# Kernel optimization log

Measured on AMD Instinct MI355X. Metric: run time of the kernel, lower is better.

The kernel has to match this reference:

```python
import jax, jax.numpy as jnp
import numpy as np

B, CIN, COUT, G = 1, 64, 64, 1
NLAT, NLON = 256, 512
LMAX, MMAX = NLAT, NLON // 2 + 1  # torch-harmonics: lmax=nlat, mmax=nlon//2+1


def _legpoly(mmax, lmax, cost):
    """Fully (ortho) normalized associated Legendre \bar P_l^m(cos t), shape [mmax, lmax, nlat]."""
    nlat = cost.shape[0]
    p = np.zeros((mmax, lmax, nlat), dtype=np.float64)
    sint = np.sqrt(1.0 - cost * cost)
    pmm = np.full(nlat, np.sqrt(1.0 / (4.0 * np.pi)))  # \bar P_0^0
    for m in range(mmax):
        if m < lmax:
            p[m, m] = pmm
        if m + 1 < lmax:
            p[m, m + 1] = np.sqrt(2.0 * m + 3.0) * cost * pmm
        for l in range(m + 2, lmax):
            a = np.sqrt((4.0 * l * l - 1.0) / (l * l - m * m))
            b = np.sqrt(((l - 1.0) ** 2 - m * m) / (4.0 * (l - 1.0) ** 2 - 1.0))
            p[m, l] = a * (cost * p[m, l - 1] - b * p[m, l - 2])
        # diagonal step: \bar P_{m+1}^{m+1}
        pmm = -np.sqrt((2.0 * m + 3.0) / (2.0 * m + 2.0)) * sint * pmm
    return p


def setup_inputs():
    key = jax.random.key(0)
    k1, k2, k3 = jax.random.split(key, 3)
    # Gauss-Legendre nodes/weights (grid='legendre-gauss')
    cost, wq = np.polynomial.legendre.leggauss(NLAT)
    pct = _legpoly(MMAX, LMAX, cost)                      # [m, l, k] - ISHT matrix
    sht_w = pct * wq[None, None, :]                        # [m, l, k] - SHT matrix (Legendre * quadrature)
    x = jax.random.normal(k1, (B, CIN, NLAT, NLON), jnp.float32)
    # weight init: scale = sqrt(1/(Cin/g)), scale[0] *= sqrt(2); complex randn has var 1/2 per component
    scale = np.full(LMAX, np.sqrt(1.0 / (CIN // G)), np.float32)
    scale[0] *= np.sqrt(2.0)
    scale = scale * np.sqrt(0.5)
    weight_r = jax.random.normal(k2, (G, CIN // G, COUT // G, LMAX), jnp.float32) * scale
    weight_i = jax.random.normal(k3, (G, CIN // G, COUT // G, LMAX), jnp.float32) * scale
    return {"x": x, "weight_r": weight_r, "weight_i": weight_i,
            "pct": jnp.asarray(pct.astype(np.float32)),
            "sht_w": jnp.asarray(sht_w.astype(np.float32))}


def reference(x, weight_r, weight_i, pct, sht_w):
    residual = x  # scale_residual is False (same in/out shape and grid)
    x = x.astype(jnp.float32)
    # --- forward real SHT: rfft over lon, Legendre transform over lat ---
    xf = 2.0 * jnp.pi * jnp.fft.rfft(x, axis=-1, norm="forward")          # [B,C,k,m] complex64
    coeffs = jnp.einsum('bckm,mlk->bclm', xf, sht_w.astype(xf.dtype))      # [B,C,l,m]
    Bd, C, L, M = coeffs.shape
    # --- grouped per-l complex weight contraction (_contract_lwise) ---
    w = (weight_r + 1j * weight_i).astype(coeffs.dtype)                    # [g,i,o,l]
    xg = coeffs.reshape(Bd, G, C // G, L, M)
    out = jnp.einsum('bgilm,giol->bgolm', xg, w).reshape(Bd, COUT, L, M)
    # --- inverse real SHT ---
    xk = jnp.einsum('bolm,mlk->bokm', out, pct.astype(out.dtype))          # [B,Cout,k,m]
    y = jnp.fft.irfft(xk, n=NLON, axis=-1, norm="forward")                 # [B,Cout,nlat,nlon]
    return (y.astype(residual.dtype), residual)
```

## Files before the change

### kernel.cpp

```cpp
#include <hip/hip_runtime.h>

typedef _Float16 f16;
typedef _Float16 h8 __attribute__((ext_vector_type(8)));
typedef float f4 __attribute__((ext_vector_type(4)));

#define NLON 512
#define NLAT 256
#define NC   64
#define NM   256
#define NL   256
#define RTOT (NC*NLAT)

#define BO_FTR 0
#define BO_FTI (BO_FTR + 262144)
#define BO_GR  (BO_FTI + 262144)
#define BO_GI  (BO_GR  + 262144)
#define BO_WTR (BO_GI  + 262144)
#define BO_WTI (BO_WTR + 2097152)
#define BO_XFRE (BO_WTI + 2097152)
#define BO_XFIM (BO_XFRE + 8388608)
#define BO_PRE  (BO_XFIM + 8388608)
#define BO_PIM  (BO_PRE + 8388608)
#define BO_QRE  (BO_PIM + 8388608)
#define BO_QIM  (BO_QRE + 8388608)
// ... 14 lines not shown
    const float sc = 6.2831853071795864769f / 512.0f;
    Ftr[idx] = (f16)(sc * cosf(th));
    Fti[idx] = (f16)(-sc * sinf(th));
  }
  {
    int n = idx >> 8, m = idx & 255;
    int t = (n * m) & (NLON - 1);
    float th = t * step;
    float s = (m == 0) ? 1.0f : 2.0f;
    Gr[idx] = (f16)(s * cosf(th));
    Gi[idx] = (f16)(-s * sinf(th));
  }
}

__global__ void k_permw2(const float* __restrict__ wr, const float* __restrict__ wi,
                         f16* __restrict__ wTr, f16* __restrict__ wTi) {
  __shared__ float tile[32][33];
  int z = blockIdx.z;
  int o = z >> 1;
  const float* w = (z & 1) ? wi : wr;
  f16* wT = (z & 1) ? wTi : wTr;
  int i0 = blockIdx.y * 32;
  int l0 = blockIdx.x * 32;
  int xx = threadIdx.x, yy = threadIdx.y;
  for (int j = 0; j < 32; j += 8)
    tile[yy + j][xx] = w[(size_t)(i0 + yy + j) * (NC * NL) + (size_t)o * NL + l0 + xx];
  __syncthreads();
  for (int j = 0; j < 32; j += 8)
    wT[(size_t)(l0 + yy + j) * (NC * NC) + (size_t)o * NC + i0 + xx] = (f16)tile[xx][yy + j];
}

__global__ __launch_bounds__(256) void k_s1(
    const float* __restrict__ x, const f16* __restrict__ Ftr,
    const f16* __restrict__ Fti, f16* __restrict__ XFre, f16* __restrict__ XFim,
    float* __restrict__ res) {
  __shared__ f16 Ar[128 * 40], Ai[128 * 40], Bx[64 * 40];
  int t = threadIdx.x;
  int m0 = blockIdx.x * 128, r0 = blockIdx.y * 64;
  int lane = t & 63, w = t >> 6;
  int wm = (w >> 1) * 32, wn = (w & 1) * 32;
  int fr = lane & 15, kg = (lane >> 4) * 8;
  int srow = t >> 2, skc = (t & 3) * 8;
  f4 aR[4][2] = {}, aI[4][2] = {};
  for (int n0 = 0; n0 < NLON; n0 += 32) {
#pragma unroll
    for (int rep = 0; rep < 2; ++rep) {
      int f = rep * 256 + t;
      int row = f >> 2, c8 = (f & 3) * 8;
      *(h8*)&Ar[row * 40 + c8] = *(const h8*)(Ftr + (size_t)(m0 + row) * NLON + n0 + c8);
      *(h8*)&Ai[row * 40 + c8] = *(const h8*)(Fti + (size_t)(m0 + row) * NLON + n0 + c8);
    }
    const float* px = x + (size_t)(r0 + srow) * NLON + n0 + skc;
    float4 v0 = *(const float4*)px;
    float4 v1 = *(const float4*)(px + 4);
    if (blockIdx.x == 0) {
      float* pr = res + (size_t)(r0 + srow) * NLON + n0 + skc;
      *(float4*)pr = v0;
      *(float4*)(pr + 4) = v1;
    }
    h8 hx = {(f16)v0.x, (f16)v0.y, (f16)v0.z, (f16)v0.w,
             (f16)v1.x, (f16)v1.y, (f16)v1.z, (f16)v1.w};
    *(h8*)&Bx[srow * 40 + skc] = hx;
    __syncthreads();
    h8 b0 = *(h8*)&Bx[(wn + fr) * 40 + kg];
    h8 b1 = *(h8*)&Bx[(wn + 16 + fr) * 40 + kg];
#pragma unroll
    for (int im = 0; im < 4; ++im) {
      int mrow = wm + (im >> 1) * 64 + (im & 1) * 16 + fr;
      h8 a = *(h8*)&Ar[mrow * 40 + kg];
      h8 c = *(h8*)&Ai[mrow * 40 + kg];
      aR[im][0] = mfma16(a, b0, aR[im][0]); aR[im][1] = mfma16(a, b1, aR[im][1]);
      aI[im][0] = mfma16(c, b0, aI[im][0]); aI[im][1] = mfma16(c, b1, aI[im][1]);
    }
    __syncthreads();
  }
  int drow = (lane >> 4) * 4, dcol = lane & 15;
#pragma unroll
  for (int im = 0; im < 4; ++im)
#pragma unroll
    for (int j = 0; j < 2; ++j)
#pragma unroll
      for (int b = 0; b < 4; ++b) {
        int mg = m0 + wm + (im >> 1) * 64 + (im & 1) * 16 + drow + b;
        size_t o = (size_t)mg * RTOT + r0 + wn + j * 16 + dcol;
        XFre[o] = (f16)aR[im][j][b];
        XFim[o] = (f16)aI[im][j][b];
      }
}

__global__ __launch_bounds__(256) void k_s2(
    const f16* __restrict__ XFre, const f16* __restrict__ XFim,
    const float* __restrict__ shtw, f16* __restrict__ Pre, f16* __restrict__ Pim) {
  int m = blockIdx.y;
  int l0 = blockIdx.x * 64;
  int t = threadIdx.x;
  if (l0 + 64 <= m) {
    h8 z = {};
#pragma unroll
    for (int rep = 0; rep < 2; ++rep) {
      int f = rep * 256 + t;
      int ll = f >> 3, c8 = (f & 7) * 8;
      size_t o = (size_t)(l0 + ll) * RTOT + (size_t)m * 64 + c8;
      *(h8*)(Pre + o) = z;
      *(h8*)(Pim + o) = z;
    }
    return;
  }
  __shared__ f16 SH[9216];
  f16* Ar = SH;
  f16* Ai = SH + 2560;
  f16* Bs = SH + 5120;
  int lane = t & 63, w = t >> 6;
  int wm = (w >> 1) * 32, wn = (w & 1) * 32;
  int fr = lane & 15, kg = (lane >> 4) * 8;
  int srow = t >> 2, skc = (t & 3) * 8;
  const f16* Abr = XFre + (size_t)m * RTOT;
  const f16* Abi = XFim + (size_t)m * RTOT;
  const float* Bb = shtw + (size_t)m * (NL * NLAT);
  f4 aR[2][2] = {}, aI[2][2] = {};
  for (int k0 = 0; k0 < NLAT; k0 += 32) {
    *(h8*)&Ar[srow * 40 + skc] = *(const h8*)(Abr + (size_t)srow * NLAT + k0 + skc);
    *(h8*)&Ai[srow * 40 + skc] = *(const h8*)(Abi + (size_t)srow * NLAT + k0 + skc);
    const float* pb = Bb + (size_t)(l0 + srow) * NLAT + k0 + skc;
    float4 v0 = *(const float4*)pb;
    float4 v1 = *(const float4*)(pb + 4);
    h8 hb = {(f16)v0.x, (f16)v0.y, (f16)v0.z, (f16)v0.w,
             (f16)v1.x, (f16)v1.y, (f16)v1.z, (f16)v1.w};
    *(h8*)&Bs[srow * 40 + skc] = hb;
    __syncthreads();
    h8 a0 = *(h8*)&Ar[(wm + fr) * 40 + kg],      a1 = *(h8*)&Ar[(wm + 16 + fr) * 40 + kg];
    h8 c0 = *(h8*)&Ai[(wm + fr) * 40 + kg],      c1 = *(h8*)&Ai[(wm + 16 + fr) * 40 + kg];
    h8 b0 = *(h8*)&Bs[(wn + fr) * 40 + kg],      b1 = *(h8*)&Bs[(wn + 16 + fr) * 40 + kg];
    aR[0][0] = mfma16(a0, b0, aR[0][0]); aR[0][1] = mfma16(a0, b1, aR[0][1]);
    aR[1][0] = mfma16(a1, b0, aR[1][0]); aR[1][1] = mfma16(a1, b1, aR[1][1]);
    aI[0][0] = mfma16(c0, b0, aI[0][0]); aI[0][1] = mfma16(c0, b1, aI[0][1]);
    aI[1][0] = mfma16(c1, b0, aI[1][0]); aI[1][1] = mfma16(c1, b1, aI[1][1]);
    __syncthreads();
  }
  f16* Tr = SH;
  f16* Ti = SH + 4608;
  int drow = (lane >> 4) * 4, dcol = lane & 15;
#pragma unroll
  for (int i = 0; i < 2; ++i)
#pragma unroll
    for (int j = 0; j < 2; ++j)
#pragma unroll
      for (int b = 0; b < 4; ++b) {
        int c = wm + i * 16 + drow + b;
        int l = wn + j * 16 + dcol;
        Tr[l * 72 + c] = (f16)aR[i][j][b];
        Ti[l * 72 + c] = (f16)aI[i][j][b];
      }
  __syncthreads();
#pragma unroll
  for (int rep = 0; rep < 4; ++rep) {
    int f = rep * 256 + t;
    int buf = f >> 9, idx = f & 511;
    int ll = idx >> 3, c8 = (idx & 7) * 8;
    const f16* T = buf ? Ti : Tr;
    h8 v = *(const h8*)&T[ll * 72 + c8];
    f16* Pd = buf ? Pim : Pre;
    *(h8*)(Pd + (size_t)(l0 + ll) * RTOT + (size_t)m * 64 + c8) = v;
  }
}

__global__ __launch_bounds__(256) void k_s3(
    const f16* __restrict__ Pre, const f16* __restrict__ Pim,
    const f16* __restrict__ wTr, const f16* __restrict__ wTi,
    f16* __restrict__ Qre, f16* __restrict__ Qim) {
  int l = blockIdx.y;
  int m0 = blockIdx.x * 64;
  int t = threadIdx.x;
  size_t obase = (size_t)l * RTOT + (size_t)m0 * 64;
  if (m0 > l) {
    h8 z = {};
#pragma unroll
    for (int rep = 0; rep < 2; ++rep) {
      int f = rep * 256 + t;
      ((h8*)(Qre + obase))[f] = z;
      ((h8*)(Qim + obase))[f] = z;
    }
    return;
  }
  __shared__ f16 SH[18432];
  f16* Ar = SH;
  f16* Ai = SH + 4608;
  f16* Br = SH + 9216;
  f16* Bi = SH + 13824;
  const f16* Pbr = Pre + (size_t)l * RTOT + (size_t)m0 * 64;
  const f16* Pbi = Pim + (size_t)l * RTOT + (size_t)m0 * 64;
  const f16* Wbr = wTr + (size_t)l * 4096;
  const f16* Wbi = wTi + (size_t)l * 4096;
#pragma unroll
  for (int rep = 0; rep < 2; ++rep) {
    int f = rep * 256 + t;
    int row = f >> 3, c8 = (f & 7) * 8;
    *(h8*)&Ar[row * 72 + c8] = *(const h8*)(Pbr + (size_t)row * 64 + c8);
    *(h8*)&Ai[row * 72 + c8] = *(const h8*)(Pbi + (size_t)row * 64 + c8);
    *(h8*)&Br[row * 72 + c8] = *(const h8*)(Wbr + (size_t)f * 8);
    *(h8*)&Bi[row * 72 + c8] = *(const h8*)(Wbi + (size_t)f * 8);
  }
  __syncthreads();
  int lane = t & 63, w = t >> 6;
  int wm = (w >> 1) * 32, wn = (w & 1) * 32;
  int fr = lane & 15, kg = (lane >> 4) * 8;
  f4 RR[2][2] = {}, II[2][2] = {}, RI[2][2] = {}, IR[2][2] = {};
#pragma unroll
  for (int ks = 0; ks < 64; ks += 32) {
    h8 a0 = *(h8*)&Ar[(wm + fr) * 72 + ks + kg];
    h8 a1 = *(h8*)&Ar[(wm + 16 + fr) * 72 + ks + kg];
    h8 c0 = *(h8*)&Ai[(wm + fr) * 72 + ks + kg];
    h8 c1 = *(h8*)&Ai[(wm + 16 + fr) * 72 + ks + kg];
    h8 b0 = *(h8*)&Br[(wn + fr) * 72 + ks + kg];
    h8 b1 = *(h8*)&Br[(wn + 16 + fr) * 72 + ks + kg];
    h8 d0 = *(h8*)&Bi[(wn + fr) * 72 + ks + kg];
    h8 d1 = *(h8*)&Bi[(wn + 16 + fr) * 72 + ks + kg];
// ... 7 lines not shown
    IR[1][0] = mfma16(c1, b0, IR[1][0]); IR[1][1] = mfma16(c1, b1, IR[1][1]);
  }
  __syncthreads();
  f16* Tr = SH;
  f16* Ti = SH + 4608;
  int drow = (lane >> 4) * 4, dcol = lane & 15;
#pragma unroll
  for (int i = 0; i < 2; ++i)
#pragma unroll
    for (int j = 0; j < 2; ++j)
#pragma unroll
      for (int b = 0; b < 4; ++b) {
        int mm = wm + i * 16 + drow + b;
        int oo = wn + j * 16 + dcol;
        Tr[mm * 72 + oo] = (f16)(RR[i][j][b] - II[i][j][b]);
        Ti[mm * 72 + oo] = (f16)(RI[i][j][b] + IR[i][j][b]);
      }
  __syncthreads();
#pragma unroll
  for (int rep = 0; rep < 4; ++rep) {
    int f = rep * 256 + t;
    int buf = f >> 9, idx = f & 511;
    int mm = idx >> 3, o8 = (idx & 7) * 8;
    const f16* T = buf ? Ti : Tr;
    h8 v = *(const h8*)&T[mm * 72 + o8];
    f16* Qd = buf ? Qim : Qre;
    *(h8*)(Qd + obase + (size_t)mm * 64 + o8) = v;
  }
}

__global__ __launch_bounds__(256) void k_s4(
    const f16* __restrict__ Qre, const f16* __restrict__ Qim,
    const float* __restrict__ pct, f16* __restrict__ XKre, f16* __restrict__ XKim) {
  __shared__ f16 As[32 * 66], Ais[32 * 66], Bs0[32 * 66], Bs1[32 * 66];
  int m = blockIdx.y;
  int k0b = blockIdx.x * 128;
  int t = threadIdx.x;
  int lane = t & 63, w = t >> 6;
  int wm = (w >> 1) * 32, wn = (w & 1) * 32;
  int fr = lane & 15, kg = (lane >> 4) * 8;
  int lr = t >> 3, c8 = (t & 7) * 8;
  const float* Bb = pct + (size_t)m * (NL * NLAT);
  f4 aR[2][4] = {}, aI[2][4] = {};
  int lstart = m & ~31;
  for (int l0 = lstart; l0 < NL; l0 += 32) {
    *(h8*)&As[lr * 66 + c8]  = *(const h8*)(Qre + (size_t)(l0 + lr) * RTOT + (size_t)m * 64 + c8);
    *(h8*)&Ais[lr * 66 + c8] = *(const h8*)(Qim + (size_t)(l0 + lr) * RTOT + (size_t)m * 64 + c8);
    const float* pb = Bb + (size_t)(l0 + lr) * NLAT + k0b + c8;
    {
      float4 v0 = *(const float4*)pb;
      float4 v1 = *(const float4*)(pb + 4);
      h8 hb = {(f16)v0.x, (f16)v0.y, (f16)v0.z, (f16)v0.w,
               (f16)v1.x, (f16)v1.y, (f16)v1.z, (f16)v1.w};
      *(h8*)&Bs0[lr * 66 + c8] = hb;
    }
    {
      float4 v0 = *(const float4*)(pb + 64);
      float4 v1 = *(const float4*)(pb + 68);
      h8 hb = {(f16)v0.x, (f16)v0.y, (f16)v0.z, (f16)v0.w,
               (f16)v1.x, (f16)v1.y, (f16)v1.z, (f16)v1.w};
      *(h8*)&Bs1[lr * 66 + c8] = hb;
    }
    __syncthreads();
    h8 a0, a1, c0, c1, b0, b1, b2, b3;
#pragma unroll
    for (int e = 0; e < 8; ++e) {
      int row = (kg + e) * 66;
      a0[e] = As[row + wm + fr];
      a1[e] = As[row + wm + 16 + fr];
      c0[e] = Ais[row + wm + fr];
      c1[e] = Ais[row + wm + 16 + fr];
      b0[e] = Bs0[row + wn + fr];
      b1[e] = Bs0[row + wn + 16 + fr];
      b2[e] = Bs1[row + wn + fr];
      b3[e] = Bs1[row + wn + 16 + fr];
    }
    aR[0][0] = mfma16(a0, b0, aR[0][0]); aR[0][1] = mfma16(a0, b1, aR[0][1]);
    aR[0][2] = mfma16(a0, b2, aR[0][2]); aR[0][3] = mfma16(a0, b3, aR[0][3]);
    aR[1][0] = mfma16(a1, b0, aR[1][0]); aR[1][1] = mfma16(a1, b1, aR[1][1]);
    aR[1][2] = mfma16(a1, b2, aR[1][2]); aR[1][3] = mfma16(a1, b3, aR[1][3]);
    aI[0][0] = mfma16(c0, b0, aI[0][0]); aI[0][1] = mfma16(c0, b1, aI[0][1]);
    aI[0][2] = mfma16(c0, b2, aI[0][2]); aI[0][3] = mfma16(c0, b3, aI[0][3]);
    aI[1][0] = mfma16(c1, b0, aI[1][0]); aI[1][1] = mfma16(c1, b1, aI[1][1]);
    aI[1][2] = mfma16(c1, b2, aI[1][2]); aI[1][3] = mfma16(c1, b3, aI[1][3]);
    __syncthreads();
  }
  int drow = (lane >> 4) * 4, dcol = lane & 15;
#pragma unroll
  for (int i = 0; i < 2; ++i)
#pragma unroll
    for (int j = 0; j < 4; ++j)
#pragma unroll
      for (int b = 0; b < 4; ++b) {
        int orow = wm + i * 16 + drow + b;
        int kcol = k0b + (j >> 1) * 64 + (j & 1) * 16 + wn + dcol;
        size_t o = (size_t)m * RTOT + (size_t)orow * NLAT + kcol;
        XKre[o] = (f16)aR[i][j][b];
        XKim[o] = (f16)aI[i][j][b];
      }
}

__global__ __launch_bounds__(256) void k_s5(
    const f16* __restrict__ XKre, const f16* __restrict__ XKim,
    const f16* __restrict__ Gr, const f16* __restrict__ Gi,
    float* __restrict__ y) {
  __shared__ f16 Ar[32 * 66], Ai[32 * 66], Br[128 * 34], Bi[128 * 34];
  int t = threadIdx.x;
  int n0 = blockIdx.x * 128, r0 = blockIdx.y * 64;
  int lane = t & 63, w = t >> 6;
  int wm = (w >> 1) * 32, wn = (w & 1) * 32;
  int fr = lane & 15, kg = (lane >> 4) * 8;
  int mr = t >> 3, r8 = (t & 7) * 8;
  f4 acc[2][4] = {};
  for (int m0 = 0; m0 < NM; m0 += 32) {
    *(h8*)&Ar[mr * 66 + r8] = *(const h8*)(XKre + (size_t)(m0 + mr) * RTOT + r0 + r8);
    *(h8*)&Ai[mr * 66 + r8] = *(const h8*)(XKim + (size_t)(m0 + mr) * RTOT + r0 + r8);
#pragma unroll
    for (int rep = 0; rep < 2; ++rep) {
      int f = rep * 256 + t;
      int row = f >> 2, cc = (f & 3) * 8;
      *(h8*)&Br[row * 34 + cc] = *(const h8*)(Gr + (size_t)(n0 + row) * NM + m0 + cc);
      *(h8*)&Bi[row * 34 + cc] = *(const h8*)(Gi + (size_t)(n0 + row) * NM + m0 + cc);
    }
    __syncthreads();
    h8 a0, a1, c0, c1;
#pragma unroll
    for (int e = 0; e < 8; ++e) {
      int row = (kg + e) * 66;
      a0[e] = Ar[row + wm + fr];
      a1[e] = Ar[row + wm + 16 + fr];
      c0[e] = Ai[row + wm + fr];
      c1[e] = Ai[row + wm + 16 + fr];
    }
#pragma unroll
    for (int j = 0; j < 4; ++j) {
      int nb = wn + (j & 1) * 16 + (j >> 1) * 64;
      h8 b = *(h8*)&Br[(nb + fr) * 34 + kg];
      h8 d = *(h8*)&Bi[(nb + fr) * 34 + kg];
      acc[0][j] = mfma16(a0, b, acc[0][j]);
      acc[1][j] = mfma16(a1, b, acc[1][j]);
      acc[0][j] = mfma16(c0, d, acc[0][j]);
      acc[1][j] = mfma16(c1, d, acc[1][j]);
    }
    __syncthreads();
  }
  int drow = (lane >> 4) * 4, dcol = lane & 15;
#pragma unroll
  for (int i = 0; i < 2; ++i)
#pragma unroll
    for (int j = 0; j < 4; ++j)
#pragma unroll
      for (int b = 0; b < 4; ++b) {
        int rg = r0 + wm + i * 16 + drow + b;
        int ng = n0 + wn + (j & 1) * 16 + (j >> 1) * 64 + dcol;
        y[(size_t)rg * NLON + ng] = acc[i][j][b];
      }
}

extern "C" void kernel_launch(void* const* d_in, const int* in_sizes, int n_in,
                              void* d_out, int out_size, void* d_ws, size_t ws_size,
                              hipStream_t stream) {
  const float* x    = (const float*)d_in[0];
  const float* wgr  = (const float*)d_in[1];
  const float* wgi  = (const float*)d_in[2];
  const float* pct  = (const float*)d_in[3];
  const float* shtw = (const float*)d_in[4];
  float* out = (float*)d_out;
  char* ws = (char*)d_ws;

  f16* Ftr = (f16*)(ws + BO_FTR);
  f16* Fti = (f16*)(ws + BO_FTI);
  f16* Gr  = (f16*)(ws + BO_GR);
  f16* Gi  = (f16*)(ws + BO_GI);
  f16* wTr = (f16*)(ws + BO_WTR);
  f16* wTi = (f16*)(ws + BO_WTI);
  f16* XFre = (f16*)(ws + BO_XFRE);
  f16* XFim = (f16*)(ws + BO_XFIM);
  f16* Pre  = (f16*)(ws + BO_PRE);
  f16* Pim  = (f16*)(ws + BO_PIM);
  f16* Qre  = (f16*)(ws + BO_QRE);
  f16* Qim  = (f16*)(ws + BO_QIM);

  float* res = out + (size_t)NC * NLAT * NLON;

  hipLaunchKernelGGL(k_tables_h, dim3(512), dim3(256), 0, stream, Ftr, Fti, Gr, Gi);
  hipLaunchKernelGGL(k_permw2, dim3(8, 2, 128), dim3(32, 8), 0, stream, wgr, wgi, wTr, wTi);
  hipLaunchKernelGGL(k_s1, dim3(2, 256), dim3(256), 0, stream, x, Ftr, Fti, XFre, XFim, res);
  hipLaunchKernelGGL(k_s2, dim3(4, 256), dim3(256), 0, stream, XFre, XFim, shtw, Pre, Pim);
  hipLaunchKernelGGL(k_s3, dim3(4, 256), dim3(256), 0, stream, Pre, Pim, wTr, wTi, Qre, Qim);
  hipLaunchKernelGGL(k_s4, dim3(2, 256), dim3(256), 0, stream, Qre, Qim, pct, XFre, XFim);
  hipLaunchKernelGGL(k_s5, dim3(4, 256), dim3(256), 0, stream, XFre, XFim, Gr, Gi, out);
}
```

Baseline: 117.0 us.

## Double-buffer shared memory with register prefetch in four GEMM stage kernels

Stages s1, s2, s4 and s5 now keep two shared-memory tile buffers. Each one loads the next K-slice from global memory into registers while MFMAs run on the current buffer, then writes the prefetched data into the other buffer. This halves the __syncthreads per iteration and is meant to hide global load latency behind compute. In exchange it doubles LDS usage and raises register pressure, which may lower occupancy.

```diff
diff --git a/kernel.cpp b/kernel.cpp
--- a/kernel.cpp
+++ b/kernel.cpp
@@ -72,45 +72,86 @@
     const float* __restrict__ x, const f16* __restrict__ Ftr,
     const f16* __restrict__ Fti, f16* __restrict__ XFre, f16* __restrict__ XFim,
     float* __restrict__ res) {
-  __shared__ f16 Ar[128 * 40], Ai[128 * 40], Bx[64 * 40];
+  __shared__ f16 SH[2 * 12800];
   int t = threadIdx.x;
   int m0 = blockIdx.x * 128, r0 = blockIdx.y * 64;
   int lane = t & 63, w = t >> 6;
   int wm = (w >> 1) * 32, wn = (w & 1) * 32;
   int fr = lane & 15, kg = (lane >> 4) * 8;
   int srow = t >> 2, skc = (t & 3) * 8;
+  int arow0 = t >> 2, ac = (t & 3) * 8;
+  int arow1 = (t + 256) >> 2;
   f4 aR[4][2] = {}, aI[4][2] = {};
-  for (int n0 = 0; n0 < NLON; n0 += 32) {
-#pragma unroll
-    for (int rep = 0; rep < 2; ++rep) {
-      int f = rep * 256 + t;
-      int row = f >> 2, c8 = (f & 3) * 8;
-      *(h8*)&Ar[row * 40 + c8] = *(const h8*)(Ftr + (size_t)(m0 + row) * NLON + n0 + c8);
-      *(h8*)&Ai[row * 40 + c8] = *(const h8*)(Fti + (size_t)(m0 + row) * NLON + n0 + c8);
-    }
-    const float* px = x + (size_t)(r0 + srow) * NLON + n0 + skc;
-    float4 v0 = *(const float4*)px;
-    float4 v1 = *(const float4*)(px + 4);
+  h8 rAr0, rAr1, rAi0, rAi1;
+  float4 rX0, rX1;
+  rAr0 = *(const h8*)(Ftr + (size_t)(m0 + arow0) * NLON + ac);
+  rAr1 = *(const h8*)(Ftr + (size_t)(m0 + arow1) * NLON + ac);
+  rAi0 = *(const h8*)(Fti + (size_t)(m0 + arow0) * NLON + ac);
+  rAi1 = *(const h8*)(Fti + (size_t)(m0 + arow1) * NLON + ac);
+  {
+    const float* px = x + (size_t)(r0 + srow) * NLON + skc;
+    rX0 = *(const float4*)px; rX1 = *(const float4*)(px + 4);
     if (blockIdx.x == 0) {
-      float* pr = res + (size_t)(r0 + srow) * NLON + n0 + skc;
-      *(float4*)pr = v0;
-      *(float4*)(pr + 4) = v1;
-    }
-    h8 hx = {(f16)v0.x, (f16)v0.y, (f16)v0.z, (f16)v0.w,
-             (f16)v1.x, (f16)v1.y, (f16)v1.z, (f16)v1.w};
+      float* pr = res + (size_t)(r0 + srow) * NLON + skc;
+      *(float4*)pr = rX0; *(float4*)(pr + 4) = rX1;
+    }
+  }
+  {
+    f16* Ar = SH; f16* Ai = SH + 5120; f16* Bx = SH + 10240;
+    *(h8*)&Ar[arow0 * 40 + ac] = rAr0;
+    *(h8*)&Ar[arow1 * 40 + ac] = rAr1;
+    *(h8*)&Ai[arow0 * 40 + ac] = rAi0;
+    *(h8*)&Ai[arow1 * 40 + ac] = rAi1;
+    h8 hx = {(f16)rX0.x, (f16)rX0.y, (f16)rX0.z, (f16)rX0.w,
+             (f16)rX1.x, (f16)rX1.y, (f16)rX1.z, (f16)rX1.w};
     *(h8*)&Bx[srow * 40 + skc] = hx;
+  }
+  __syncthreads();
+  int cur = 0;
+  for (int it = 0; it < 16; ++it) {
+    bool more = (it + 1) < 16;
+    if (more) {
+      int n0 = (it + 1) * 32;
+      rAr0 = *(const h8*)(Ftr + (size_t)(m0 + arow0) * NLON + n0 + ac);
+      rAr1 = *(const h8*)(Ftr + (size_t)(m0 + arow1) * NLON + n0 + ac);
+      rAi0 = *(const h8*)(Fti + (size_t)(m0 + arow0) * NLON + n0 + ac);
+      rAi1 = *(const h8*)(Fti + (size_t)(m0 + arow1) * NLON + n0 + ac);
+      const float* px = x + (size_t)(r0 + srow) * NLON + n0 + skc;
+      rX0 = *(const float4*)px; rX1 = *(const float4*)(px + 4);
+      if (blockIdx.x == 0) {
+        float* pr = res + (size_t)(r0 + srow) * NLON + n0 + skc;
+        *(float4*)pr = rX0; *(float4*)(pr + 4) = rX1;
+      }
+    }
+    {
+      const f16* Ar = SH + cur * 12800;
+      const f16* Ai = Ar + 5120;
+      const f16* Bx = Ar + 10240;
+      h8 b0 = *(const h8*)&Bx[(wn + fr) * 40 + kg];
+      h8 b1 = *(const h8*)&Bx[(wn + 16 + fr) * 40 + kg];
+#pragma unroll
+      for (int im = 0; im < 4; ++im) {
+        int mrow = wm + (im >> 1) * 64 + (im & 1) * 16 + fr;
+        h8 a = *(const h8*)&Ar[mrow * 40 + kg];
+        h8 c = *(const h8*)&Ai[mrow * 40 + kg];
+        aR[im][0] = mfma16(a, b0, aR[im][0]); aR[im][1] = mfma16(a, b1, aR[im][1]);
+        aI[im][0] = mfma16(c, b0, aI[im][0]); aI[im][1] = mfma16(c, b1, aI[im][1]);
+      }
+    }
+    if (more) {
+      f16* Ar = SH + (cur ^ 1) * 12800;
+      f16* Ai = Ar + 5120;
+      f16* Bx = Ar + 10240;
+      *(h8*)&Ar[arow0 * 40 + ac] = rAr0;
+      *(h8*)&Ar[arow1 * 40 + ac] = rAr1;
+      *(h8*)&Ai[arow0 * 40 + ac] = rAi0;
+      *(h8*)&Ai[arow1 * 40 + ac] = rAi1;
+      h8 hx = {(f16)rX0.x, (f16)rX0.y, (f16)rX0.z, (f16)rX0.w,
+               (f16)rX1.x, (f16)rX1.y, (f16)rX1.z, (f16)rX1.w};
+      *(h8*)&Bx[srow * 40 + skc] = hx;
+    }
     __syncthreads();
-    h8 b0 = *(h8*)&Bx[(wn + fr) * 40 + kg];
-    h8 b1 = *(h8*)&Bx[(wn + 16 + fr) * 40 + kg];
-#pragma unroll
-    for (int im = 0; im < 4; ++im) {
-      int mrow = wm + (im >> 1) * 64 + (im & 1) * 16 + fr;
-      h8 a = *(h8*)&Ar[mrow * 40 + kg];
-      h8 c = *(h8*)&Ai[mrow * 40 + kg];
-      aR[im][0] = mfma16(a, b0, aR[im][0]); aR[im][1] = mfma16(a, b1, aR[im][1]);
-      aI[im][0] = mfma16(c, b0, aI[im][0]); aI[im][1] = mfma16(c, b1, aI[im][1]);
-    }
-    __syncthreads();
+    cur ^= 1;
   }
   int drow = (lane >> 4) * 4, dcol = lane & 15;
 #pragma unroll
@@ -130,24 +171,21 @@
     const f16* __restrict__ XFre, const f16* __restrict__ XFim,
     const float* __restrict__ shtw, f16* __restrict__ Pre, f16* __restrict__ Pim) {
   int m = blockIdx.y;
-  int l0 = blockIdx.x * 64;
+  int l0b = blockIdx.x * 64;
   int t = threadIdx.x;
-  if (l0 + 64 <= m) {
+  if (l0b + 64 <= m) {
     h8 z = {};
 #pragma unroll
     for (int rep = 0; rep < 2; ++rep) {
       int f = rep * 256 + t;
       int ll = f >> 3, c8 = (f & 7) * 8;
-      size_t o = (size_t)(l0 + ll) * RTOT + (size_t)m * 64 + c8;
+      size_t o = (size_t)(l0b + ll) * RTOT + (size_t)m * 64 + c8;
       *(h8*)(Pre + o) = z;
       *(h8*)(Pim + o) = z;
     }
     return;
   }
-  __shared__ f16 SH[9216];
-  f16* Ar = SH;
-  f16* Ai = SH + 2560;
-  f16* Bs = SH + 5120;
+  __shared__ f16 SH[2 * 7680];
   int lane = t & 63, w = t >> 6;
   int wm = (w >> 1) * 32, wn = (w & 1) * 32;
   int fr = lane & 15, kg = (lane >> 4) * 8;
@@ -156,24 +194,57 @@
   const f16* Abi = XFim + (size_t)m * RTOT;
   const float* Bb = shtw + (size_t)m * (NL * NLAT);
   f4 aR[2][2] = {}, aI[2][2] = {};
-  for (int k0 = 0; k0 < NLAT; k0 += 32) {
-    *(h8*)&Ar[srow * 40 + skc] = *(const h8*)(Abr + (size_t)srow * NLAT + k0 + skc);
-    *(h8*)&Ai[srow * 40 + skc] = *(const h8*)(Abi + (size_t)srow * NLAT + k0 + skc);
-    const float* pb = Bb + (size_t)(l0 + srow) * NLAT + k0 + skc;
-    float4 v0 = *(const float4*)pb;
-    float4 v1 = *(const float4*)(pb + 4);
-    h8 hb = {(f16)v0.x, (f16)v0.y, (f16)v0.z, (f16)v0.w,
-             (f16)v1.x, (f16)v1.y, (f16)v1.z, (f16)v1.w};
+  h8 rA, rAi;
+  float4 rB0, rB1;
+  rA  = *(const h8*)(Abr + (size_t)srow * NLAT + skc);
+  rAi = *(const h8*)(Abi + (size_t)srow * NLAT + skc);
+  {
+    const float* pb = Bb + (size_t)(l0b + srow) * NLAT + skc;
+    rB0 = *(const float4*)pb; rB1 = *(const float4*)(pb + 4);
+  }
+  {
+    f16* Ar = SH; f16* Ai = SH + 2560; f16* Bs = SH + 5120;
+    *(h8*)&Ar[srow * 40 + skc] = rA;
+    *(h8*)&Ai[srow * 40 + skc] = rAi;
+    h8 hb = {(f16)rB0.x, (f16)rB0.y, (f16)rB0.z, (f16)rB0.w,
+             (f16)rB1.x, (f16)rB1.y, (f16)rB1.z, (f16)rB1.w};
     *(h8*)&Bs[srow * 40 + skc] = hb;
+  }
+  __syncthreads();
+  int cur = 0;
+  for (int it = 0; it < 8; ++it) {
+    bool more = (it + 1) < 8;
+    if (more) {
+      int k0 = (it + 1) * 32;
+      rA  = *(const h8*)(Abr + (size_t)srow * NLAT + k0 + skc);
+      rAi = *(const h8*)(Abi + (size_t)srow * NLAT + k0 + skc);
+      const float* pb = Bb + (size_t)(l0b + srow) * NLAT + k0 + skc;
+      rB0 = *(const float4*)pb; rB1 = *(const float4*)(pb + 4);
+    }
+    {
+      const f16* Ar = SH + cur * 7680;
+      const f16* Ai = Ar + 2560;
+      const f16* Bs = Ar + 5120;
+      h8 a0 = *(const h8*)&Ar[(wm + fr) * 40 + kg],      a1 = *(const h8*)&Ar[(wm + 16 + fr) * 40 + kg];
+      h8 c0 = *(const h8*)&Ai[(wm + fr) * 40 + kg],      c1 = *(const h8*)&Ai[(wm + 16 + fr) * 40 + kg];
+      h8 b0 = *(const h8*)&Bs[(wn + fr) * 40 + kg],      b1 = *(const h8*)&Bs[(wn + 16 + fr) * 40 + kg];
+      aR[0][0] = mfma16(a0, b0, aR[0][0]); aR[0][1] = mfma16(a0, b1, aR[0][1]);
+      aR[1][0] = mfma16(a1, b0, aR[1][0]); aR[1][1] = mfma16(a1, b1, aR[1][1]);
+      aI[0][0] = mfma16(c0, b0, aI[0][0]); aI[0][1] = mfma16(c0, b1, aI[0][1]);
+      aI[1][0] = mfma16(c1, b0, aI[1][0]); aI[1][1] = mfma16(c1, b1, aI[1][1]);
+    }
+    if (more) {
+      f16* Ar = SH + (cur ^ 1) * 7680;
+      f16* Ai = Ar + 2560;
+      f16* Bs = Ar + 5120;
+      *(h8*)&Ar[srow * 40 + skc] = rA;
+      *(h8*)&Ai[srow * 40 + skc] = rAi;
+      h8 hb = {(f16)rB0.x, (f16)rB0.y, (f16)rB0.z, (f16)rB0.w,
+               (f16)rB1.x, (f16)rB1.y, (f16)rB1.z, (f16)rB1.w};
+      *(h8*)&Bs[srow * 40 + skc] = hb;
+    }
     __syncthreads();
-    h8 a0 = *(h8*)&Ar[(wm + fr) * 40 + kg],      a1 = *(h8*)&Ar[(wm + 16 + fr) * 40 + kg];
-    h8 c0 = *(h8*)&Ai[(wm + fr) * 40 + kg],      c1 = *(h8*)&Ai[(wm + 16 + fr) * 40 + kg];
-    h8 b0 = *(h8*)&Bs[(wn + fr) * 40 + kg],      b1 = *(h8*)&Bs[(wn + 16 + fr) * 40 + kg];
-    aR[0][0] = mfma16(a0, b0, aR[0][0]); aR[0][1] = mfma16(a0, b1, aR[0][1]);
-    aR[1][0] = mfma16(a1, b0, aR[1][0]); aR[1][1] = mfma16(a1, b1, aR[1][1]);
-    aI[0][0] = mfma16(c0, b0, aI[0][0]); aI[0][1] = mfma16(c0, b1, aI[0][1]);
-    aI[1][0] = mfma16(c1, b0, aI[1][0]); aI[1][1] = mfma16(c1, b1, aI[1][1]);
-    __syncthreads();
+    cur ^= 1;
   }
   f16* Tr = SH;
   f16* Ti = SH + 4608;
@@ -198,7 +269,7 @@
     const f16* T = buf ? Ti : Tr;
     h8 v = *(const h8*)&T[ll * 72 + c8];
     f16* Pd = buf ? Pim : Pre;
-    *(h8*)(Pd + (size_t)(l0 + ll) * RTOT + (size_t)m * 64 + c8) = v;
+    *(h8*)(Pd + (size_t)(l0b + ll) * RTOT + (size_t)m * 64 + c8) = v;
   }
 }
 
@@ -293,7 +364,7 @@
 __global__ __launch_bounds__(256) void k_s4(
     const f16* __restrict__ Qre, const f16* __restrict__ Qim,
     const float* __restrict__ pct, f16* __restrict__ XKre, f16* __restrict__ XKim) {
-  __shared__ f16 As[32 * 66], Ais[32 * 66], Bs0[32 * 66], Bs1[32 * 66];
+  __shared__ f16 SH[2 * 8448];
   int m = blockIdx.y;
   int k0b = blockIdx.x * 128;
   int t = threadIdx.x;
@@ -304,47 +375,82 @@
   const float* Bb = pct + (size_t)m * (NL * NLAT);
   f4 aR[2][4] = {}, aI[2][4] = {};
   int lstart = m & ~31;
-  for (int l0 = lstart; l0 < NL; l0 += 32) {
-    *(h8*)&As[lr * 66 + c8]  = *(const h8*)(Qre + (size_t)(l0 + lr) * RTOT + (size_t)m * 64 + c8);
-    *(h8*)&Ais[lr * 66 + c8] = *(const h8*)(Qim + (size_t)(l0 + lr) * RTOT + (size_t)m * 64 + c8);
-    const float* pb = Bb + (size_t)(l0 + lr) * NLAT + k0b + c8;
+  int nt = (NL - lstart) >> 5;
+  h8 rQr, rQi;
+  float4 rP0, rP1, rP2, rP3;
+  rQr = *(const h8*)(Qre + (size_t)(lstart + lr) * RTOT + (size_t)m * 64 + c8);
+  rQi = *(const h8*)(Qim + (size_t)(lstart + lr) * RTOT + (size_t)m * 64 + c8);
+  {
+    const float* pb = Bb + (size_t)(lstart + lr) * NLAT + k0b + c8;
+    rP0 = *(const float4*)pb;       rP1 = *(const float4*)(pb + 4);
+    rP2 = *(const float4*)(pb + 64); rP3 = *(const float4*)(pb + 68);
+  }
+  {
+    f16* As = SH; f16* Ais = SH + 2112; f16* Bs0 = SH + 4224; f16* Bs1 = SH + 6336;
+    *(h8*)&As[lr * 66 + c8] = rQr;
+    *(h8*)&Ais[lr * 66 + c8] = rQi;
+    h8 h0 = {(f16)rP0.x, (f16)rP0.y, (f16)rP0.z, (f16)rP0.w,
+             (f16)rP1.x, (f16)rP1.y, (f16)rP1.z, (f16)rP1.w};
+    h8 h1 = {(f16)rP2.x, (f16)rP2.y, (f16)rP2.z, (f16)rP2.w,
+             (f16)rP3.x, (f16)rP3.y, (f16)rP3.z, (f16)rP3.w};
+    *(h8*)&Bs0[lr * 66 + c8] = h0;
+    *(h8*)&Bs1[lr * 66 + c8] = h1;
+  }
+  __syncthreads();
+  int cur = 0;
+  for (int it = 0; it < nt; ++it) {
+    bool more = (it + 1) < nt;
+    if (more) {
+      int l0 = lstart + (it + 1) * 32;
+      rQr = *(const h8*)(Qre + (size_t)(l0 + lr) * RTOT + (size_t)m * 64 + c8);
+      rQi = *(const h8*)(Qim + (size_t)(l0 + lr) * RTOT + (size_t)m * 64 + c8);
+      const float* pb = Bb + (size_t)(l0 + lr) * NLAT + k0b + c8;
+      rP0 = *(const float4*)pb;       rP1 = *(const float4*)(pb + 4);
+      rP2 = *(const float4*)(pb + 64); rP3 = *(const float4*)(pb + 68);
+    }
     {
-      float4 v0 = *(const float4*)pb;
-      float4 v1 = *(const float4*)(pb + 4);
-      h8 hb = {(f16)v0.x, (f16)v0.y, (f16)v0.z, (f16)v0.w,
-               (f16)v1.x, (f16)v1.y, (f16)v1.z, (f16)v1.w};
-      *(h8*)&Bs0[lr * 66 + c8] = hb;
-    }
-    {
-      float4 v0 = *(const float4*)(pb + 64);
-      float4 v1 = *(const float4*)(pb + 68);
-      h8 hb = {(f16)v0.x, (f16)v0.y, (f16)v0.z, (f16)v0.w,
-               (f16)v1.x, (f16)v1.y, (f16)v1.z, (f16)v1.w};
-      *(h8*)&Bs1[lr * 66 + c8] = hb;
+      const f16* As = SH + cur * 8448;
+      const f16* Ais = As + 2112;
+      const f16* Bs0 = As + 4224;
+      const f16* Bs1 = As + 6336;
+      h8 a0, a1, c0, c1, b0, b1, b2, b3;
+#pragma unroll
+      for (int e = 0; e < 8; ++e) {
+        int row = (kg + e) * 66;
+        a0[e] = As[row + wm + fr];
+        a1[e] = As[row + wm + 16 + fr];
+        c0[e] = Ais[row + wm + fr];
+        c1[e] = Ais[row + wm + 16 + fr];
+        b0[e] = Bs0[row + wn + fr];
+        b1[e] = Bs0[row + wn + 16 + fr];
+        b2[e] = Bs1[row + wn + fr];
+        b3[e] = Bs1[row + wn + 16 + fr];
+      }
+      aR[0][0] = mfma16(a0, b0, aR[0][0]); aR[0][1] = mfma16(a0, b1, aR[0][1]);
+      aR[0][2] = mfma16(a0, b2, aR[0][2]); aR[0][3] = mfma16(a0, b3, aR[0][3]);
+      aR[1][0] = mfma16(a1, b0, aR[1][0]); aR[1][1] = mfma16(a1, b1, aR[1][1]);
+      aR[1][2] = mfma16(a1, b2, aR[1][2]); aR[1][3] = mfma16(a1, b3, aR[1][3]);
+      aI[0][0] = mfma16(c0, b0, aI[0][0]); aI[0][1] = mfma16(c0, b1, aI[0][1]);
+      aI[0][2] = mfma16(c0, b2, aI[0][2]); aI[0][3] = mfma16(c0, b3, aI[0][3]);
+      aI[1][0] = mfma16(c1, b0, aI[1][0]); aI[1][1] = mfma16(c1, b1, aI[1][1]);
+      aI[1][2] = mfma16(c1, b2, aI[1][2]); aI[1][3] = mfma16(c1, b3, aI[1][3]);
+    }
+    if (more) {
+      f16* As = SH + (cur ^ 1) * 8448;
+      f16* Ais = As + 2112;
+      f16* Bs0 = As + 4224;
+      f16* Bs1 = As + 6336;
+      *(h8*)&As[lr * 66 + c8] = rQr;
+      *(h8*)&Ais[lr * 66 + c8] = rQi;
+      h8 h0 = {(f16)rP0.x, (f16)rP0.y, (f16)rP0.z, (f16)rP0.w,
+               (f16)rP1.x, (f16)rP1.y, (f16)rP1.z, (f16)rP1.w};
+      h8 h1 = {(f16)rP2.x, (f16)rP2.y, (f16)rP2.z, (f16)rP2.w,
+               (f16)rP3.x, (f16)rP3.y, (f16)rP3.z, (f16)rP3.w};
+      *(h8*)&Bs0[lr * 66 + c8] = h0;
+      *(h8*)&Bs1[lr * 66 + c8] = h1;
     }
     __syncthreads();
-    h8 a0, a1, c0, c1, b0, b1, b2, b3;
-#pragma unroll
-    for (int e = 0; e < 8; ++e) {
-      int row = (kg + e) * 66;
-      a0[e] = As[row + wm + fr];
-      a1[e] = As[row + wm + 16 + fr];
-      c0[e] = Ais[row + wm + fr];
-      c1[e] = Ais[row + wm + 16 + fr];
-      b0[e] = Bs0[row + wn + fr];
-      b1[e] = Bs0[row + wn + 16 + fr];
-      b2[e] = Bs1[row + wn + fr];
-      b3[e] = Bs1[row + wn + 16 + fr];
-    }
-    aR[0][0] = mfma16(a0, b0, aR[0][0]); aR[0][1] = mfma16(a0, b1, aR[0][1]);
-    aR[0][2] = mfma16(a0, b2, aR[0][2]); aR[0][3] = mfma16(a0, b3, aR[0][3]);
-    aR[1][0] = mfma16(a1, b0, aR[1][0]); aR[1][1] = mfma16(a1, b1, aR[1][1]);
-    aR[1][2] = mfma16(a1, b2, aR[1][2]); aR[1][3] = mfma16(a1, b3, aR[1][3]);
-    aI[0][0] = mfma16(c0, b0, aI[0][0]); aI[0][1] = mfma16(c0, b1, aI[0][1]);
-    aI[0][2] = mfma16(c0, b2, aI[0][2]); aI[0][3] = mfma16(c0, b3, aI[0][3]);
-    aI[1][0] = mfma16(c1, b0, aI[1][0]); aI[1][1] = mfma16(c1, b1, aI[1][1]);
-    aI[1][2] = mfma16(c1, b2, aI[1][2]); aI[1][3] = mfma16(c1, b3, aI[1][3]);
-    __syncthreads();
+    cur ^= 1;
   }
   int drow = (lane >> 4) * 4, dcol = lane & 15;
 #pragma unroll
@@ -365,45 +471,84 @@
     const f16* __restrict__ XKre, const f16* __restrict__ XKim,
     const f16* __restrict__ Gr, const f16* __restrict__ Gi,
     float* __restrict__ y) {
-  __shared__ f16 Ar[32 * 66], Ai[32 * 66], Br[128 * 34], Bi[128 * 34];
+  __shared__ f16 SH[2 * 12928];
   int t = threadIdx.x;
   int n0 = blockIdx.x * 128, r0 = blockIdx.y * 64;
   int lane = t & 63, w = t >> 6;
   int wm = (w >> 1) * 32, wn = (w & 1) * 32;
   int fr = lane & 15, kg = (lane >> 4) * 8;
   int mr = t >> 3, r8 = (t & 7) * 8;
+  int brow0 = t >> 2, bc = (t & 3) * 8;
+  int brow1 = (t + 256) >> 2;
   f4 acc[2][4] = {};
-  for (int m0 = 0; m0 < NM; m0 += 32) {
-    *(h8*)&Ar[mr * 66 + r8] = *(const h8*)(XKre + (size_t)(m0 + mr) * RTOT + r0 + r8);
-    *(h8*)&Ai[mr * 66 + r8] = *(const h8*)(XKim + (size_t)(m0 + mr) * RTOT + r0 + r8);
-#pragma unroll
-    for (int rep = 0; rep < 2; ++rep) {
-      int f = rep * 256 + t;
-      int row = f >> 2, cc = (f & 3) * 8;
-      *(h8*)&Br[row * 34 + cc] = *(const h8*)(Gr + (size_t)(n0 + row) * NM + m0 + cc);
-      *(h8*)&Bi[row * 34 + cc] = *(const h8*)(Gi + (size_t)(n0 + row) * NM + m0 + cc);
+  h8 rXr, rXi, rG0, rG1, rH0, rH1;
+  rXr = *(const h8*)(XKre + (size_t)mr * RTOT + r0 + r8);
+  rXi = *(const h8*)(XKim + (size_t)mr * RTOT + r0 + r8);
+  rG0 = *(const h8*)(Gr + (size_t)(n0 + brow0) * NM + bc);
+  rG1 = *(const h8*)(Gr + (size_t)(n0 + brow1) * NM + bc);
+  rH0 = *(const h8*)(Gi + (size_t)(n0 + brow0) * NM + bc);
+  rH1 = *(const h8*)(Gi + (size_t)(n0 + brow1) * NM + bc);
+  {
+    f16* Ar = SH; f16* Ai = SH + 2112; f16* Br = SH + 4224; f16* Bi = SH + 8576;
+    *(h8*)&Ar[mr * 66 + r8] = rXr;
+    *(h8*)&Ai[mr * 66 + r8] = rXi;
+    *(h8*)&Br[brow0 * 34 + bc] = rG0;
+    *(h8*)&Br[brow1 * 34 + bc] = rG1;
+    *(h8*)&Bi[brow0 * 34 + bc] = rH0;
+    *(h8*)&Bi[brow1 * 34 + bc] = rH1;
+  }
+  __syncthreads();
+  int cur = 0;
+  for (int it = 0; it < 8; ++it) {
+    bool more = (it + 1) < 8;
+    if (more) {
+      int m0 = (it + 1) * 32;
+      rXr = *(const h8*)(XKre + (size_t)(m0 + mr) * RTOT + r0 + r8);
+      rXi = *(const h8*)(XKim + (size_t)(m0 + mr) * RTOT + r0 + r8);
+      rG0 = *(const h8*)(Gr + (size_t)(n0 + brow0) * NM + m0 + bc);
+      rG1 = *(const h8*)(Gr + (size_t)(n0 + brow1) * NM + m0 + bc);
+      rH0 = *(const h8*)(Gi + (size_t)(n0 + brow0) * NM + m0 + bc);
+      rH1 = *(const h8*)(Gi + (size_t)(n0 + brow1) * NM + m0 + bc);
+    }
+    {
+      const f16* Ar = SH + cur * 12928;
+      const f16* Ai = Ar + 2112;
+      const f16* Br = Ar + 4224;
+      const f16* Bi = Ar + 8576;
+      h8 a0, a1, c0, c1;
+#pragma unroll
+      for (int e = 0; e < 8; ++e) {
+        int row = (kg + e) * 66;
+        a0[e] = Ar[row + wm + fr];
+        a1[e] = Ar[row + wm + 16 + fr];
+        c0[e] = Ai[row + wm + fr];
+        c1[e] = Ai[row + wm + 16 + fr];
+      }
+#pragma unroll
+      for (int j = 0; j < 4; ++j) {
+        int nb = wn + (j & 1) * 16 + (j >> 1) * 64;
+        h8 b = *(const h8*)&Br[(nb + fr) * 34 + kg];
+        h8 d = *(const h8*)&Bi[(nb + fr) * 34 + kg];
+        acc[0][j] = mfma16(a0, b, acc[0][j]);
+        acc[1][j] = mfma16(a1, b, acc[1][j]);
+        acc[0][j] = mfma16(c0, d, acc[0][j]);
+        acc[1][j] = mfma16(c1, d, acc[1][j]);
+      }
+    }
+    if (more) {
+      f16* Ar = SH + (cur ^ 1) * 12928;
+      f16* Ai = Ar + 2112;
+      f16* Br = Ar + 4224;
+      f16* Bi = Ar + 8576;
+      *(h8*)&Ar[mr * 66 + r8] = rXr;
+      *(h8*)&Ai[mr * 66 + r8] = rXi;
+      *(h8*)&Br[brow0 * 34 + bc] = rG0;
+      *(h8*)&Br[brow1 * 34 + bc] = rG1;
+      *(h8*)&Bi[brow0 * 34 + bc] = rH0;
+      *(h8*)&Bi[brow1 * 34 + bc] = rH1;
     }
     __syncthreads();
-    h8 a0, a1, c0, c1;
-#pragma unroll
-    for (int e = 0; e < 8; ++e) {
-      int row = (kg + e) * 66;
-      a0[e] = Ar[row + wm + fr];
-      a1[e] = Ar[row + wm + 16 + fr];
-      c0[e] = Ai[row + wm + fr];
-      c1[e] = Ai[row + wm + 16 + fr];
-    }
-#pragma unroll
-    for (int j = 0; j < 4; ++j) {
-      int nb = wn + (j & 1) * 16 + (j >> 1) * 64;
-      h8 b = *(h8*)&Br[(nb + fr) * 34 + kg];
-      h8 d = *(h8*)&Bi[(nb + fr) * 34 + kg];
-      acc[0][j] = mfma16(a0, b, acc[0][j]);
-      acc[1][j] = mfma16(a1, b, acc[1][j]);
-      acc[0][j] = mfma16(c0, d, acc[0][j]);
-      acc[1][j] = mfma16(c1, d, acc[1][j]);
-    }
-    __syncthreads();
+    cur ^= 1;
   }
   int drow = (lane >> 4) * 4, dcol = lane & 15;
 #pragma unroll
```

New measurement: 149.0 us. 1.27x slower.

## Double-buffer LDS tiles with register prefetch in forward DFT GEMM kernel

Applied to the files above, without the earlier changes.

Restructures the k_s1 (longitude DFT as GEMM) main loop to use two shared-memory buffers and prefetch the next k-slice of DFT matrices and input into registers while MFMAs run on the current buffer. This removes one __syncthreads per iteration and lets global load latency overlap with compute. It doubles LDS use per block, which may reduce occupancy, and adds register pressure.

```diff
diff --git a/kernel.cpp b/kernel.cpp
--- a/kernel.cpp
+++ b/kernel.cpp
@@ -72,45 +72,86 @@
     const float* __restrict__ x, const f16* __restrict__ Ftr,
     const f16* __restrict__ Fti, f16* __restrict__ XFre, f16* __restrict__ XFim,
     float* __restrict__ res) {
-  __shared__ f16 Ar[128 * 40], Ai[128 * 40], Bx[64 * 40];
+  __shared__ f16 SH[2 * 12800];
   int t = threadIdx.x;
   int m0 = blockIdx.x * 128, r0 = blockIdx.y * 64;
   int lane = t & 63, w = t >> 6;
   int wm = (w >> 1) * 32, wn = (w & 1) * 32;
   int fr = lane & 15, kg = (lane >> 4) * 8;
   int srow = t >> 2, skc = (t & 3) * 8;
+  int arow0 = t >> 2, ac = (t & 3) * 8;
+  int arow1 = (t + 256) >> 2;
   f4 aR[4][2] = {}, aI[4][2] = {};
-  for (int n0 = 0; n0 < NLON; n0 += 32) {
-#pragma unroll
-    for (int rep = 0; rep < 2; ++rep) {
-      int f = rep * 256 + t;
-      int row = f >> 2, c8 = (f & 3) * 8;
-      *(h8*)&Ar[row * 40 + c8] = *(const h8*)(Ftr + (size_t)(m0 + row) * NLON + n0 + c8);
-      *(h8*)&Ai[row * 40 + c8] = *(const h8*)(Fti + (size_t)(m0 + row) * NLON + n0 + c8);
-    }
-    const float* px = x + (size_t)(r0 + srow) * NLON + n0 + skc;
-    float4 v0 = *(const float4*)px;
-    float4 v1 = *(const float4*)(px + 4);
+  h8 rAr0, rAr1, rAi0, rAi1;
+  float4 rX0, rX1;
+  rAr0 = *(const h8*)(Ftr + (size_t)(m0 + arow0) * NLON + ac);
+  rAr1 = *(const h8*)(Ftr + (size_t)(m0 + arow1) * NLON + ac);
+  rAi0 = *(const h8*)(Fti + (size_t)(m0 + arow0) * NLON + ac);
+  rAi1 = *(const h8*)(Fti + (size_t)(m0 + arow1) * NLON + ac);
+  {
+    const float* px = x + (size_t)(r0 + srow) * NLON + skc;
+    rX0 = *(const float4*)px; rX1 = *(const float4*)(px + 4);
     if (blockIdx.x == 0) {
-      float* pr = res + (size_t)(r0 + srow) * NLON + n0 + skc;
-      *(float4*)pr = v0;
-      *(float4*)(pr + 4) = v1;
-    }
-    h8 hx = {(f16)v0.x, (f16)v0.y, (f16)v0.z, (f16)v0.w,
-             (f16)v1.x, (f16)v1.y, (f16)v1.z, (f16)v1.w};
+      float* pr = res + (size_t)(r0 + srow) * NLON + skc;
+      *(float4*)pr = rX0; *(float4*)(pr + 4) = rX1;
+    }
+  }
+  {
+    f16* Ar = SH; f16* Ai = SH + 5120; f16* Bx = SH + 10240;
+    *(h8*)&Ar[arow0 * 40 + ac] = rAr0;
+    *(h8*)&Ar[arow1 * 40 + ac] = rAr1;
+    *(h8*)&Ai[arow0 * 40 + ac] = rAi0;
+    *(h8*)&Ai[arow1 * 40 + ac] = rAi1;
+    h8 hx = {(f16)rX0.x, (f16)rX0.y, (f16)rX0.z, (f16)rX0.w,
+             (f16)rX1.x, (f16)rX1.y, (f16)rX1.z, (f16)rX1.w};
     *(h8*)&Bx[srow * 40 + skc] = hx;
-    __syncthreads();
-    h8 b0 = *(h8*)&Bx[(wn + fr) * 40 + kg];
-    h8 b1 = *(h8*)&Bx[(wn + 16 + fr) * 40 + kg];
-#pragma unroll
-    for (int im = 0; im < 4; ++im) {
-      int mrow = wm + (im >> 1) * 64 + (im & 1) * 16 + fr;
-      h8 a = *(h8*)&Ar[mrow * 40 + kg];
-      h8 c = *(h8*)&Ai[mrow * 40 + kg];
-      aR[im][0] = mfma16(a, b0, aR[im][0]); aR[im][1] = mfma16(a, b1, aR[im][1]);
-      aI[im][0] = mfma16(c, b0, aI[im][0]); aI[im][1] = mfma16(c, b1, aI[im][1]);
-    }
-    __syncthreads();
+  }
+  __syncthreads();
+  int cur = 0;
+  for (int it = 0; it < 16; ++it) {
+    bool more = (it + 1) < 16;
+    if (more) {
+      int n0 = (it + 1) * 32;
+      rAr0 = *(const h8*)(Ftr + (size_t)(m0 + arow0) * NLON + n0 + ac);
+      rAr1 = *(const h8*)(Ftr + (size_t)(m0 + arow1) * NLON + n0 + ac);
+      rAi0 = *(const h8*)(Fti + (size_t)(m0 + arow0) * NLON + n0 + ac);
+      rAi1 = *(const h8*)(Fti + (size_t)(m0 + arow1) * NLON + n0 + ac);
+      const float* px = x + (size_t)(r0 + srow) * NLON + n0 + skc;
+      rX0 = *(const float4*)px; rX1 = *(const float4*)(px + 4);
+      if (blockIdx.x == 0) {
+        float* pr = res + (size_t)(r0 + srow) * NLON + n0 + skc;
+        *(float4*)pr = rX0; *(float4*)(pr + 4) = rX1;
+      }
+    }
+    {
+      const f16* Ar = SH + cur * 12800;
+      const f16* Ai = Ar + 5120;
+      const f16* Bx = Ar + 10240;
+      h8 b0 = *(const h8*)&Bx[(wn + fr) * 40 + kg];
+      h8 b1 = *(const h8*)&Bx[(wn + 16 + fr) * 40 + kg];
+#pragma unroll
+      for (int im = 0; im < 4; ++im) {
+        int mrow = wm + (im >> 1) * 64 + (im & 1) * 16 + fr;
+        h8 a = *(const h8*)&Ar[mrow * 40 + kg];
+        h8 c = *(const h8*)&Ai[mrow * 40 + kg];
+        aR[im][0] = mfma16(a, b0, aR[im][0]); aR[im][1] = mfma16(a, b1, aR[im][1]);
+        aI[im][0] = mfma16(c, b0, aI[im][0]); aI[im][1] = mfma16(c, b1, aI[im][1]);
+      }
+    }
+    if (more) {
+      f16* Ar = SH + (cur ^ 1) * 12800;
+      f16* Ai = Ar + 5120;
+      f16* Bx = Ar + 10240;
+      *(h8*)&Ar[arow0 * 40 + ac] = rAr0;
+      *(h8*)&Ar[arow1 * 40 + ac] = rAr1;
+      *(h8*)&Ai[arow0 * 40 + ac] = rAi0;
+      *(h8*)&Ai[arow1 * 40 + ac] = rAi1;
+      h8 hx = {(f16)rX0.x, (f16)rX0.y, (f16)rX0.z, (f16)rX0.w,
+               (f16)rX1.x, (f16)rX1.y, (f16)rX1.z, (f16)rX1.w};
+      *(h8*)&Bx[srow * 40 + skc] = hx;
+    }
+    __syncthreads();
+    cur ^= 1;
   }
   int drow = (lane >> 4) * 4, dcol = lane & 15;
 #pragma unroll
```

New measurement: 116.7 us. About the same (-0.2%).

## Coalesce k_s1 stores via LDS, drop zero-fills, move residual copy to k_s5

Applied to the files above, without the earlier changes.

The k_s1 epilogue now stages each accumulator plane through shared memory and writes XF with 16-byte coalesced row stores, replacing scattered 2-byte stores. The k_s2 and k_s3 blocks that cover the zero triangle now return early instead of writing zeros to P and Q, which removes that store traffic. The residual copy of x moves out of the k_s1 main loop into a coalesced float4 tail in k_s5. Dropping the zero-fills assumes later stages never read those untouched workspace regions.

```diff
diff --git a/kernel.cpp b/kernel.cpp
--- a/kernel.cpp
+++ b/kernel.cpp
@@ -70,15 +70,15 @@
 
 __global__ __launch_bounds__(256) void k_s1(
     const float* __restrict__ x, const f16* __restrict__ Ftr,
-    const f16* __restrict__ Fti, f16* __restrict__ XFre, f16* __restrict__ XFim,
-    float* __restrict__ res) {
-  __shared__ f16 Ar[128 * 40], Ai[128 * 40], Bx[64 * 40];
+    const f16* __restrict__ Fti, f16* __restrict__ XFre, f16* __restrict__ XFim) {
+  __shared__ f16 SH[12800];
   int t = threadIdx.x;
   int m0 = blockIdx.x * 128, r0 = blockIdx.y * 64;
   int lane = t & 63, w = t >> 6;
   int wm = (w >> 1) * 32, wn = (w & 1) * 32;
   int fr = lane & 15, kg = (lane >> 4) * 8;
   int srow = t >> 2, skc = (t & 3) * 8;
+  f16* Ar = SH; f16* Ai = SH + 5120; f16* Bx = SH + 10240;
   f4 aR[4][2] = {}, aI[4][2] = {};
   for (int n0 = 0; n0 < NLON; n0 += 32) {
 #pragma unroll
@@ -91,11 +91,6 @@
     const float* px = x + (size_t)(r0 + srow) * NLON + n0 + skc;
     float4 v0 = *(const float4*)px;
     float4 v1 = *(const float4*)(px + 4);
-    if (blockIdx.x == 0) {
-      float* pr = res + (size_t)(r0 + srow) * NLON + n0 + skc;
-      *(float4*)pr = v0;
-      *(float4*)(pr + 4) = v1;
-    }
     h8 hx = {(f16)v0.x, (f16)v0.y, (f16)v0.z, (f16)v0.w,
              (f16)v1.x, (f16)v1.y, (f16)v1.z, (f16)v1.w};
     *(h8*)&Bx[srow * 40 + skc] = hx;
@@ -112,18 +107,30 @@
     }
     __syncthreads();
   }
+  f16* T = SH;
   int drow = (lane >> 4) * 4, dcol = lane & 15;
 #pragma unroll
-  for (int im = 0; im < 4; ++im)
-#pragma unroll
-    for (int j = 0; j < 2; ++j)
-#pragma unroll
-      for (int b = 0; b < 4; ++b) {
-        int mg = m0 + wm + (im >> 1) * 64 + (im & 1) * 16 + drow + b;
-        size_t o = (size_t)mg * RTOT + r0 + wn + j * 16 + dcol;
-        XFre[o] = (f16)aR[im][j][b];
-        XFim[o] = (f16)aI[im][j][b];
-      }
+  for (int plane = 0; plane < 2; ++plane) {
+#pragma unroll
+    for (int im = 0; im < 4; ++im)
+#pragma unroll
+      for (int j = 0; j < 2; ++j)
+#pragma unroll
+        for (int b = 0; b < 4; ++b) {
+          int mrow = wm + (im >> 1) * 64 + (im & 1) * 16 + drow + b;
+          int rcol = wn + j * 16 + dcol;
+          T[mrow * 68 + rcol] = plane ? (f16)aI[im][j][b] : (f16)aR[im][j][b];
+        }
+    __syncthreads();
+    f16* XF = plane ? XFim : XFre;
+#pragma unroll
+    for (int rep = 0; rep < 4; ++rep) {
+      int f = rep * 256 + t;
+      int mrow = f >> 3, rc8 = (f & 7) * 8;
+      *(h8*)(XF + (size_t)(m0 + mrow) * RTOT + r0 + rc8) = *(const h8*)&T[mrow * 68 + rc8];
+    }
+    __syncthreads();
+  }
 }
 
 __global__ __launch_bounds__(256) void k_s2(
@@ -132,18 +139,7 @@
   int m = blockIdx.y;
   int l0 = blockIdx.x * 64;
   int t = threadIdx.x;
-  if (l0 + 64 <= m) {
-    h8 z = {};
-#pragma unroll
-    for (int rep = 0; rep < 2; ++rep) {
-      int f = rep * 256 + t;
-      int ll = f >> 3, c8 = (f & 7) * 8;
-      size_t o = (size_t)(l0 + ll) * RTOT + (size_t)m * 64 + c8;
-      *(h8*)(Pre + o) = z;
-      *(h8*)(Pim + o) = z;
-    }
-    return;
-  }
+  if (l0 + 64 <= m) return;
   __shared__ f16 SH[9216];
   f16* Ar = SH;
   f16* Ai = SH + 2560;
@@ -210,16 +206,7 @@
   int m0 = blockIdx.x * 64;
   int t = threadIdx.x;
   size_t obase = (size_t)l * RTOT + (size_t)m0 * 64;
-  if (m0 > l) {
-    h8 z = {};
-#pragma unroll
-    for (int rep = 0; rep < 2; ++rep) {
-      int f = rep * 256 + t;
-      ((h8*)(Qre + obase))[f] = z;
-      ((h8*)(Qim + obase))[f] = z;
-    }
-    return;
-  }
+  if (m0 > l) return;
   __shared__ f16 SH[18432];
   f16* Ar = SH;
   f16* Ai = SH + 4608;
@@ -364,7 +351,7 @@
 __global__ __launch_bounds__(256) void k_s5(
     const f16* __restrict__ XKre, const f16* __restrict__ XKim,
     const f16* __restrict__ Gr, const f16* __restrict__ Gi,
-    float* __restrict__ y) {
+    const float* __restrict__ x, float* __restrict__ y, float* __restrict__ res) {
   __shared__ f16 Ar[32 * 66], Ai[32 * 66], Br[128 * 34], Bi[128 * 34];
   int t = threadIdx.x;
   int n0 = blockIdx.x * 128, r0 = blockIdx.y * 64;
@@ -416,6 +403,13 @@
         int ng = n0 + wn + (j & 1) * 16 + (j >> 1) * 64 + dcol;
         y[(size_t)rg * NLON + ng] = acc[i][j][b];
       }
+#pragma unroll
+  for (int i = 0; i < 8; ++i) {
+    int f = i * 256 + t;
+    int row = f >> 5, c4 = (f & 31) * 4;
+    float4 v = *(const float4*)(x + (size_t)(r0 + row) * NLON + n0 + c4);
+    *(float4*)(res + (size_t)(r0 + row) * NLON + n0 + c4) = v;
+  }
 }
 
 extern "C" void kernel_launch(void* const* d_in, const int* in_sizes, int n_in,
@@ -446,9 +440,9 @@
 
   hipLaunchKernelGGL(k_tables_h, dim3(512), dim3(256), 0, stream, Ftr, Fti, Gr, Gi);
   hipLaunchKernelGGL(k_permw2, dim3(8, 2, 128), dim3(32, 8), 0, stream, wgr, wgi, wTr, wTi);
-  hipLaunchKernelGGL(k_s1, dim3(2, 256), dim3(256), 0, stream, x, Ftr, Fti, XFre, XFim, res);
+  hipLaunchKernelGGL(k_s1, dim3(2, 256), dim3(256), 0, stream, x, Ftr, Fti, XFre, XFim);
   hipLaunchKernelGGL(k_s2, dim3(4, 256), dim3(256), 0, stream, XFre, XFim, shtw, Pre, Pim);
   hipLaunchKernelGGL(k_s3, dim3(4, 256), dim3(256), 0, stream, Pre, Pim, wTr, wTi, Qre, Qim);
   hipLaunchKernelGGL(k_s4, dim3(2, 256), dim3(256), 0, stream, Qre, Qim, pct, XFre, XFim);
-  hipLaunchKernelGGL(k_s5, dim3(4, 256), dim3(256), 0, stream, XFre, XFim, Gr, Gi, out);
-}
+  hipLaunchKernelGGL(k_s5, dim3(4, 256), dim3(256), 0, stream, XFre, XFim, Gr, Gi, x, out, res);
+}
```

New measurement: 124.4 us. +6.4%, slower.
